# Kernel optimization log

Hardware: AMD Instinct MI355X
Metric: run time of the kernel (lower is better)

## Reference

```python
import jax, jax.numpy as jnp
import numpy as np

B, NQ, NK, D, DV = 8, 2048, 2048, 64, 64
MASK_VAL = -1e9  # any value < -1.0 triggers substitution in the original t.where


def setup_inputs() -> dict:
    key = jax.random.key(0)
    kq, kk, kv = jax.random.split(key, 3)
    queries = jax.random.normal(kq, (B, NQ, D), dtype=jnp.float32)
    keys = jax.random.normal(kk, (B, NK, D), dtype=jnp.float32)
    values = jax.random.normal(kv, (B, NK, DV), dtype=jnp.float32)
    # causal-style substitution mask: 0.0 where attended, -1e9 where masked
    causal = jnp.tril(jnp.ones((NQ, NK), dtype=jnp.float32))
    mask2d = jnp.where(causal > 0, 0.0, MASK_VAL)
    attention_mask = jnp.broadcast_to(mask2d, (B, NQ, NK))
    return {"queries": queries, "keys": keys, "values": values,
            "attention_mask": attention_mask}


def reference(queries, keys, values, attention_mask):
    # logits = Q K^T / sqrt(d_k)
    d_k = keys.shape[-1]
    scale = jnp.asarray(1.0 / np.sqrt(d_k), dtype=queries.dtype)
    logits = jnp.einsum('bqd,bkd->bqk', queries, keys) * scale
    # substitution masking: replace logits by the mask VALUE where mask < -1.0
    masked = jnp.where(attention_mask < -1.0, attention_mask, logits)
    attn = jax.nn.softmax(masked, axis=-1)
    # post-hoc NaN zeroing (rows fully masked with -inf would be NaN)
    attn = jnp.where(jnp.isnan(attn), jnp.asarray(0.0, attn.dtype), attn)
    return jnp.einsum('bqk,bkv->bqv', attn, values)
```

## Files before the change

### kernel.cpp

```cpp
#include <hip/hip_runtime.h>

#define NB    8
#define NQL   2048
#define NKL   2048
#define DD    64
#define DVV   64
#define QT    64
#define NQT   32
#define KSTEP 64
#define PPB   119
#define MAXCH 7

typedef __attribute__((ext_vector_type(8))) short bf16x8;
typedef __attribute__((ext_vector_type(4))) short bf16x4;
typedef __attribute__((ext_vector_type(2))) short bf16x2;
typedef __attribute__((ext_vector_type(4))) float f32x4;

#define L2E 1.44269504088896340736f

__device__ __forceinline__ unsigned short f2bf(float x) {
    union { float f; unsigned u; } v; v.f = x;
    unsigned r = v.u + 0x7FFFu + ((v.u >> 16) & 1u);
    return (unsigned short)(r >> 16);
}

__device__ __forceinline__ int kswz(int row, int col) {
    return row * 64 + (col ^ ((row & 7) << 3));
}
__device__ __forceinline__ int vswz(int dv, int col) {
    return dv * 64 + (col ^ ((((dv & 7) ^ ((dv >> 3) & 7))) << 3));
}

__global__ __launch_bounds__(256, 4)
void attn_part(const float* __restrict__ Qg, const float* __restrict__ Kg,
               const float* __restrict__ Vg, float* __restrict__ Og,
               float* __restrict__ Mp, float* __restrict__ Lp,
               float* __restrict__ Op)
{
    const int bid = blockIdx.x;
    const int b   = bid / PPB;
    const int r   = bid - b * PPB;
    int qt = 0, P = 1, j = 0;
    {
        int cum = 0;
#pragma unroll
        for (int t = 0; t < 32; ++t) {
            int pc = (t + 5) / 5;
            if (r >= cum && r < cum + pc) { qt = t; P = pc; j = r - cum; }
            cum += pc;
        }
    }
    const int n    = qt + 1;
    const int base = n / P;
    const int rem  = n - base * P;
    const int s0   = j * base + (j < rem ? j : rem);
    const int nsteps = base + (j < rem ? 1 : 0);
    const int KC0  = s0 * KSTEP;
    const int pidx = b * PPB + r;

    const int tid  = threadIdx.x;
    const int wv   = tid >> 6;
    const int lane = tid & 63;
    const int c    = lane & 15;
    const int h    = lane >> 4;
    const int Q0   = qt * QT;
    const int R0l  = 16 * wv;

    const float* Qb = Qg + (size_t)b * NQL * DD;
    const float* Kb = Kg + (size_t)b * NKL * DD;
    const float* Vb = Vg + (size_t)b * NKL * DVV;

    __shared__ short Kl[2][64 * 64];
    __shared__ short Vl[2][64 * 64];

    const int skr = tid >> 2;
    const int sdc = (tid & 3) * 16;
    const int vkr = (tid >> 3) << 1;
    const int vdc = (tid & 7) * 8;
    f32x4 kr[4], vr[4];

    bf16x8 qf[2];
#pragma unroll
    for (int dh = 0; dh < 2; ++dh) {
        const float* src = Qb + (size_t)(Q0 + R0l + c) * DD + dh * 32 + h * 8;
        f32x4 x0 = *(const f32x4*)(src);
        f32x4 x1 = *(const f32x4*)(src + 4);
        bf16x8 t;
#pragma unroll
        for (int jj = 0; jj < 4; ++jj) {
            t[jj]     = (short)f2bf(x0[jj] * 0.125f);
            t[4 + jj] = (short)f2bf(x1[jj] * 0.125f);
        }
        qf[dh] = t;
    }

    {
        const float* kb0 = Kb + (size_t)(KC0 + skr) * DD + sdc;
        kr[0] = *(const f32x4*)(kb0);     kr[1] = *(const f32x4*)(kb0 + 4);
        kr[2] = *(const f32x4*)(kb0 + 8); kr[3] = *(const f32x4*)(kb0 + 12);
        const float* vb0 = Vb + (size_t)(KC0 + vkr) * DVV + vdc;
        vr[0] = *(const f32x4*)(vb0);       vr[1] = *(const f32x4*)(vb0 + 4);
        vr[2] = *(const f32x4*)(vb0 + DVV); vr[3] = *(const f32x4*)(vb0 + DVV + 4);
        short* Kd = Kl[0]; short* Vd = Vl[0];
#pragma unroll
        for (int i = 0; i < 4; ++i) {
            bf16x4 t;
#pragma unroll
            for (int jj = 0; jj < 4; ++jj) t[jj] = (short)f2bf(kr[i][jj]);
            *(bf16x4*)(Kd + kswz(skr, sdc + 4 * i)) = t;
        }
#pragma unroll
        for (int jj = 0; jj < 8; ++jj) {
            bf16x2 t;
            t[0] = (short)f2bf(vr[jj >> 2][jj & 3]);
            t[1] = (short)f2bf(vr[2 + (jj >> 2)][jj & 3]);
            *(bf16x2*)(Vd + vswz(vdc + jj, vkr)) = t;
        }
    }
    __syncthreads();

    float m = -INFINITY, l = 0.0f;
    f32x4 acc[4];
    {
        f32x4 z = {0.f, 0.f, 0.f, 0.f};
#pragma unroll
        for (int s4 = 0; s4 < 4; ++s4) acc[s4] = z;
    }

    for (int s = 0; s < nsteps; ++s) {
        const int pb = s & 1;

        if (s + 1 < nsteps) {
            const float* kb0 = Kb + (size_t)(KC0 + (s + 1) * KSTEP + skr) * DD + sdc;
            kr[0] = *(const f32x4*)(kb0);     kr[1] = *(const f32x4*)(kb0 + 4);
            kr[2] = *(const f32x4*)(kb0 + 8); kr[3] = *(const f32x4*)(kb0 + 12);
            const float* vb0 = Vb + (size_t)(KC0 + (s + 1) * KSTEP + vkr) * DVV + vdc;
            vr[0] = *(const f32x4*)(vb0);       vr[1] = *(const f32x4*)(vb0 + 4);
            vr[2] = *(const f32x4*)(vb0 + DVV); vr[3] = *(const f32x4*)(vb0 + DVV + 4);
        }

        const int kg0 = KC0 + s * KSTEP;
        if (kg0 <= Q0 + R0l + 15) {
            const short* Kd = Kl[pb];
            const short* Vd = Vl[pb];

            f32x4 st[4];
            {
                f32x4 z = {0.f, 0.f, 0.f, 0.f};
#pragma unroll
                for (int t = 0; t < 4; ++t) st[t] = z;
            }
            __builtin_amdgcn_s_setprio(1);
#pragma unroll
            for (int t = 0; t < 4; ++t)
#pragma unroll
                for (int dh = 0; dh < 2; ++dh) {
                    bf16x8 kf = *(const bf16x8*)(Kd + kswz(16 * t + c, dh * 32 + h * 8));
                    st[t] = __builtin_amdgcn_mfma_f32_16x16x32_bf16(kf, qf[dh], st[t], 0, 0, 0);
                }
            __builtin_amdgcn_s_setprio(0);

            if (kg0 + KSTEP - 1 > Q0 + R0l) {
                const int qg = Q0 + R0l + c;
#pragma unroll
                for (int t = 0; t < 4; ++t)
#pragma unroll
                    for (int rr = 0; rr < 4; ++rr) {
                        int key = kg0 + 16 * t + 4 * h + rr;
                        if (key > qg) st[t][rr] = -1e9f;
                    }
            }

            float vmax = st[0][0];
#pragma unroll
            for (int t = 0; t < 4; ++t)
#pragma unroll
                for (int rr = 0; rr < 4; ++rr) vmax = fmaxf(vmax, st[t][rr]);
            vmax = fmaxf(vmax, __shfl_xor(vmax, 16));
            vmax = fmaxf(vmax, __shfl_xor(vmax, 32));

            if (!__all(vmax - m <= 8.0f)) {
                float mn    = fmaxf(m, vmax);
                float alpha = exp2f((m - mn) * L2E);
                l *= alpha;
#pragma unroll
                for (int s4 = 0; s4 < 4; ++s4)
#pragma unroll
                    for (int rr = 0; rr < 4; ++rr) acc[s4][rr] *= alpha;
                m = mn;
            }

            float p[4][4];
            float ps = 0.f;
#pragma unroll
            for (int t = 0; t < 4; ++t)
#pragma unroll
                for (int rr = 0; rr < 4; ++rr) {
                    p[t][rr] = exp2f((st[t][rr] - m) * L2E);
                    ps += p[t][rr];
                }
            ps += __shfl_xor(ps, 16);
            ps += __shfl_xor(ps, 32);
            l += ps;

            bf16x8 pf[2];
#pragma unroll
            for (int u = 0; u < 2; ++u) {
                bf16x8 t;
#pragma unroll
                for (int jj = 0; jj < 8; ++jj) t[jj] = (short)f2bf(p[2 * u + (jj >> 2)][jj & 3]);
                pf[u] = t;
            }
            __builtin_amdgcn_s_setprio(1);
#pragma unroll
            for (int s4 = 0; s4 < 4; ++s4)
#pragma unroll
                for (int u = 0; u < 2; ++u) {
                    bf16x4 lo = *(const bf16x4*)(Vd + vswz(c + 16 * s4, 32 * u + 4 * h));
                    bf16x4 hi = *(const bf16x4*)(Vd + vswz(c + 16 * s4, 32 * u + 16 + 4 * h));
                    bf16x8 vf = {lo[0], lo[1], lo[2], lo[3], hi[0], hi[1], hi[2], hi[3]};
                    acc[s4] = __builtin_amdgcn_mfma_f32_16x16x32_bf16(vf, pf[u], acc[s4], 0, 0, 0);
                }
            __builtin_amdgcn_s_setprio(0);
        }

        if (s + 1 < nsteps) {
            short* Kd = Kl[(s + 1) & 1];
            short* Vd = Vl[(s + 1) & 1];
#pragma unroll
            for (int i = 0; i < 4; ++i) {
                bf16x4 t;
#pragma unroll
                for (int jj = 0; jj < 4; ++jj) t[jj] = (short)f2bf(kr[i][jj]);
                *(bf16x4*)(Kd + kswz(skr, sdc + 4 * i)) = t;
            }
#pragma unroll
            for (int jj = 0; jj < 8; ++jj) {
                bf16x2 t;
                t[0] = (short)f2bf(vr[jj >> 2][jj & 3]);
                t[1] = (short)f2bf(vr[2 + (jj >> 2)][jj & 3]);
                *(bf16x2*)(Vd + vswz(vdc + jj, vkr)) = t;
            }
            __syncthreads();
        }
    }

    const int q = R0l + c;
    if (P == 1) {
        const float iv = 1.0f / l;
        float* dst = Og + ((size_t)b * NQL + Q0 + q) * DVV;
#pragma unroll
        for (int s4 = 0; s4 < 4; ++s4) {
            f32x4 t = acc[s4];
#pragma unroll
            for (int rr = 0; rr < 4; ++rr) t[rr] *= iv;
            *(f32x4*)(dst + 16 * s4 + 4 * h) = t;
        }
        return;
    }

    float* Opg = Op + (size_t)pidx * (QT * DVV);
#pragma unroll
    for (int s4 = 0; s4 < 4; ++s4)
        *(f32x4*)(Opg + (size_t)q * DVV + 16 * s4 + 4 * h) = acc[s4];
    if (h == 0) {
        Mp[(size_t)pidx * QT + q] = m;
        Lp[(size_t)pidx * QT + q] = l;
    }
}

__global__ __launch_bounds__(256)
void attn_comb(const float* __restrict__ Op, const float* __restrict__ Mp,
               const float* __restrict__ Lp, float* __restrict__ Og)
{
    const int seg = blockIdx.x & 1;
    const int t2  = blockIdx.x >> 1;
    const int b   = t2 / 27;
    const int qt  = 5 + (t2 - b * 27);
    const int nch = (qt + 5) / 5;
    int rbase = 0;
#pragma unroll
    for (int t = 0; t < 32; ++t) if (t < qt) rbase += (t + 5) / 5;
    const size_t p0 = (size_t)(b * PPB + rbase);

    const int tid = threadIdx.x;
    const int r0  = seg * 32;

    __shared__ float scb[MAXCH][32];

    if (tid < 32) {
        const int row = r0 + tid;
        float M = -INFINITY;
        for (int ch = 0; ch < nch; ++ch)
            M = fmaxf(M, Mp[(p0 + ch) * QT + row]);
        float den = 0.f;
        for (int ch = 0; ch < nch; ++ch) {
            float e = exp2f((Mp[(p0 + ch) * QT + row] - M) * L2E);
            den += e * Lp[(p0 + ch) * QT + row];
            scb[ch][tid] = e;
        }
        float iv = 1.0f / den;
        for (int ch = 0; ch < nch; ++ch) scb[ch][tid] *= iv;
    }
    __syncthreads();

    const float* Opt = Op + p0 * (QT * DVV) + (size_t)r0 * DVV;
    float* dst = Og + ((size_t)b * NQL + qt * QT + r0) * DVV;
#pragma unroll
    for (int jj = 0; jj < 8; ++jj) {
        int f = jj * 256 + tid;
        int row = f >> 6;
        float val = 0.f;
        for (int ch = 0; ch < nch; ++ch)
            val += scb[ch][row] * Opt[(size_t)ch * (QT * DVV) + f];
        dst[f] = val;
    }
}

__global__ __launch_bounds__(256, 4)
void attn_fwd_fb(const float* __restrict__ Qg, const float* __restrict__ Kg,
                 const float* __restrict__ Vg, float* __restrict__ Og)
{
    const int tid  = threadIdx.x;
    const int wv   = tid >> 6;
    const int lane = tid & 63;
    const int c    = lane & 15;
    const int h    = lane >> 4;
    const int bid = blockIdx.x;
    const int b   = bid & 7;
    const int qt  = bid >> 3;
    const int q0  = qt << 4;
    const float* Qb = Qg + (size_t)b * NQL * DD;
    const float* Kb = Kg + (size_t)b * NKL * DD;
    const float* Vb = Vg + (size_t)b * NKL * DVV;
    bf16x8 qf[2];
#pragma unroll
    for (int dh = 0; dh < 2; ++dh) {
        const float* src = Qb + (size_t)(q0 + c) * DD + dh * 32 + h * 8;
        f32x4 x0 = *(const f32x4*)(src);
        f32x4 x1 = *(const f32x4*)(src + 4);
        bf16x8 t;
#pragma unroll
        for (int jj = 0; jj < 4; ++jj) {
            t[jj]     = (short)f2bf(x0[jj] * 0.125f);
            t[4 + jj] = (short)f2bf(x1[jj] * 0.125f);
        }
        qf[dh] = t;
    }
    float m = -INFINITY, l = 0.0f;
    f32x4 acc[4];
    {
        f32x4 z = {0.f, 0.f, 0.f, 0.f};
#pragma unroll
        for (int s = 0; s < 4; ++s) acc[s] = z;
    }
    const int nkt = (q0 + 47) >> 5;
    for (int kt = wv; kt < nkt; kt += 4) {
        const int kb = kt << 5;
        f32x4 st[2];
        {
            f32x4 z = {0.f, 0.f, 0.f, 0.f};
            st[0] = z; st[1] = z;
        }
#pragma unroll
        for (int t = 0; t < 2; ++t)
#pragma unroll
            for (int dh = 0; dh < 2; ++dh) {
                const float* src = Kb + (size_t)(kb + t * 16 + c) * DD + dh * 32 + h * 8;
                f32x4 x0 = *(const f32x4*)(src);
                f32x4 x1 = *(const f32x4*)(src + 4);
                bf16x8 kf;
#pragma unroll
                for (int jj = 0; jj < 4; ++jj) {
                    kf[jj]     = (short)f2bf(x0[jj]);
                    kf[4 + jj] = (short)f2bf(x1[jj]);
                }
                st[t] = __builtin_amdgcn_mfma_f32_16x16x32_bf16(kf, qf[dh], st[t], 0, 0, 0);
            }
        if (kb + 31 > q0) {
#pragma unroll
            for (int t = 0; t < 2; ++t)
#pragma unroll
                for (int rr = 0; rr < 4; ++rr) {
                    int key = kb + t * 16 + h * 4 + rr;
                    if (key > q0 + c) st[t][rr] = -1e9f;
                }
        }
        float vmax = st[0][0];
#pragma unroll
        for (int t = 0; t < 2; ++t)
#pragma unroll
            for (int rr = 0; rr < 4; ++rr) vmax = fmaxf(vmax, st[t][rr]);
        vmax = fmaxf(vmax, __shfl_xor(vmax, 16));
        vmax = fmaxf(vmax, __shfl_xor(vmax, 32));
        float mn    = fmaxf(m, vmax);
        float alpha = exp2f((m - mn) * L2E);
        float p[2][4];
        float ps = 0.f;
#pragma unroll
        for (int t = 0; t < 2; ++t)
#pragma unroll
            for (int rr = 0; rr < 4; ++rr) {
                p[t][rr] = exp2f((st[t][rr] - mn) * L2E);
                ps += p[t][rr];
            }
        ps += __shfl_xor(ps, 16);
        ps += __shfl_xor(ps, 32);
        l = l * alpha + ps;
        m = mn;
#pragma unroll
        for (int s = 0; s < 4; ++s)
#pragma unroll
            for (int rr = 0; rr < 4; ++rr) acc[s][rr] *= alpha;
        bf16x8 pf;
#pragma unroll
        for (int jj = 0; jj < 8; ++jj) pf[jj] = (short)f2bf(p[jj >> 2][jj & 3]);
        size_t vrow[8];
#pragma unroll
        for (int jj = 0; jj < 8; ++jj)
            vrow[jj] = (size_t)(kb + h * 4 + (jj & 3) + ((jj >> 2) << 4)) * DVV + c;
#pragma unroll
        for (int s = 0; s < 4; ++s) {
            bf16x8 vf;
#pragma unroll
            for (int jj = 0; jj < 8; ++jj) vf[jj] = (short)f2bf(Vb[vrow[jj] + s * 16]);
            acc[s] = __builtin_amdgcn_mfma_f32_16x16x32_bf16(vf, pf, acc[s], 0, 0, 0);
        }
    }
    __shared__ float Osc[4][64][17];
    __shared__ float Msc[4][16];
    __shared__ float Lsc[4][16];
#pragma unroll
    for (int s = 0; s < 4; ++s)
#pragma unroll
        for (int rr = 0; rr < 4; ++rr)
            Osc[wv][s * 16 + h * 4 + rr][c] = acc[s][rr];
    if (lane < 16) { Msc[wv][c] = m; Lsc[wv][c] = l; }
    __syncthreads();
#pragma unroll
    for (int ri = 0; ri < 4; ++ri) {
        const int q = wv * 4 + ri;
        float M = fmaxf(fmaxf(Msc[0][q], Msc[1][q]), fmaxf(Msc[2][q], Msc[3][q]));
        float val = 0.f, den = 0.f;
#pragma unroll
        for (int w2 = 0; w2 < 4; ++w2) {
            float sc = exp2f((Msc[w2][q] - M) * L2E);
            den += Lsc[w2][q] * sc;
            val += Osc[w2][lane][q] * sc;
        }
        Og[((size_t)b * NQL + q0 + q) * DVV + lane] = val / den;
    }
}

extern "C" void kernel_launch(void* const* d_in, const int* in_sizes, int n_in,
                              void* d_out, int out_size, void* d_ws, size_t ws_size,
                              hipStream_t stream)
{
    (void)in_sizes; (void)n_in; (void)out_size;
    const float* Q = (const float*)d_in[0];
    const float* K = (const float*)d_in[1];
    const float* V = (const float*)d_in[2];
    float* O = (float*)d_out;

    const size_t npieces  = (size_t)NB * PPB;
    const size_t ml_elems = npieces * QT;
    const size_t op_elems = npieces * QT * DVV;
    const size_t need = (2 * ml_elems + op_elems) * sizeof(float);

    if (ws_size >= need) {
        float* Mp = (float*)d_ws;
        float* Lp = Mp + ml_elems;
        float* Op = Lp + ml_elems;
        attn_part<<<dim3(NB * PPB), dim3(256), 0, stream>>>(
            Q, K, V, O, Mp, Lp, Op);
        attn_comb<<<dim3(NB * 27 * 2), dim3(256), 0, stream>>>(Op, Mp, Lp, O);
    } else {
        attn_fwd_fb<<<dim3(NB * (NQL / 16)), dim3(256), 0, stream>>>(Q, K, V, O);
    }
}
```

Baseline: 50.12 us.

## Pre-convert K/V to bf16 (V transposed) and deepen register prefetch pipeline

Adds a pre-pass kernel that converts K to bf16 and transposes V to bf16 in workspace, so the attention kernel loads half as many bytes per tile and skips per-tile conversion and scattered V stores. The main loop is fully unrolled to a max of 5 steps with a two-stage register prefetch, and explicit vmcnt/lgkmcnt waits plus raw barriers replace __syncthreads. This adds an extra kernel launch and a full pass over K/V each call. It also relies on hand-placed waitcnt instructions being correct.

Measured after the change: 49.95 us. Within noise of the previous version (-0.3%).

```diff
diff --git a/kernel.cpp b/kernel.cpp
--- a/kernel.cpp
+++ b/kernel.cpp
@@ -10,13 +10,18 @@
 #define KSTEP 64
 #define PPB   119
 #define MAXCH 7
+#define MAXST 5
 
 typedef __attribute__((ext_vector_type(8))) short bf16x8;
 typedef __attribute__((ext_vector_type(4))) short bf16x4;
-typedef __attribute__((ext_vector_type(2))) short bf16x2;
+typedef __attribute__((ext_vector_type(8))) unsigned short u16x8;
 typedef __attribute__((ext_vector_type(4))) float f32x4;
 
 #define L2E 1.44269504088896340736f
+
+#define VMCNT4 asm volatile("s_waitcnt vmcnt(4)" ::: "memory")
+#define VMCNT0 asm volatile("s_waitcnt vmcnt(0)" ::: "memory")
+#define LGKM0  asm volatile("s_waitcnt lgkmcnt(0)" ::: "memory")
 
 __device__ __forceinline__ unsigned short f2bf(float x) {
     union { float f; unsigned u; } v; v.f = x;
@@ -31,9 +36,47 @@
     return dv * 64 + (col ^ ((((dv & 7) ^ ((dv >> 3) & 7))) << 3));
 }
 
+__global__ __launch_bounds__(256)
+void cvt_kv(const float* __restrict__ K, const float* __restrict__ V,
+            unsigned short* __restrict__ Kw, unsigned short* __restrict__ Vt)
+{
+    const int bid = blockIdx.x;
+    if (bid < 512) {
+        size_t i = ((size_t)bid * 256 + threadIdx.x) * 8;
+        f32x4 a = *(const f32x4*)(K + i);
+        f32x4 b = *(const f32x4*)(K + i + 4);
+        u16x8 o;
+#pragma unroll
+        for (int j = 0; j < 4; ++j) { o[j] = f2bf(a[j]); o[4 + j] = f2bf(b[j]); }
+        *(u16x8*)(Kw + i) = o;
+    } else {
+        const int v  = bid - 512;
+        const int b  = v >> 5;
+        const int k0 = (v & 31) << 6;
+        __shared__ float tile[64][65];
+        const float* Vb = V + ((size_t)b * NKL + k0) * DVV;
+        const int col = threadIdx.x & 63;
+        const int r4  = threadIdx.x >> 6;
+#pragma unroll
+        for (int i = 0; i < 16; ++i) {
+            int r = i * 4 + r4;
+            tile[r][col] = Vb[(size_t)r * DVV + col];
+        }
+        __syncthreads();
+        unsigned short* Vtb = Vt + (size_t)b * DVV * NKL;
+#pragma unroll
+        for (int i = 0; i < 16; ++i) {
+            int dv = i * 4 + r4;
+            Vtb[(size_t)dv * NKL + k0 + col] = f2bf(tile[col][dv]);
+        }
+    }
+}
+
 __global__ __launch_bounds__(256, 4)
-void attn_part(const float* __restrict__ Qg, const float* __restrict__ Kg,
-               const float* __restrict__ Vg, float* __restrict__ Og,
+void attn_part(const float* __restrict__ Qg,
+               const unsigned short* __restrict__ Kw,
+               const unsigned short* __restrict__ Vt,
+               float* __restrict__ Og,
                float* __restrict__ Mp, float* __restrict__ Lp,
                float* __restrict__ Op)
 {
@@ -50,13 +93,13 @@
             cum += pc;
         }
     }
-    const int n    = qt + 1;
-    const int base = n / P;
-    const int rem  = n - base * P;
-    const int s0   = j * base + (j < rem ? j : rem);
+    const int n      = qt + 1;
+    const int base   = n / P;
+    const int rem    = n - base * P;
+    const int s0     = j * base + (j < rem ? j : rem);
     const int nsteps = base + (j < rem ? 1 : 0);
-    const int KC0  = s0 * KSTEP;
-    const int pidx = b * PPB + r;
+    const int KC0    = s0 * KSTEP;
+    const int pidx   = b * PPB + r;
 
     const int tid  = threadIdx.x;
     const int wv   = tid >> 6;
@@ -66,18 +109,33 @@
     const int Q0   = qt * QT;
     const int R0l  = 16 * wv;
 
-    const float* Qb = Qg + (size_t)b * NQL * DD;
-    const float* Kb = Kg + (size_t)b * NKL * DD;
-    const float* Vb = Vg + (size_t)b * NKL * DVV;
+    const float*          Qb  = Qg + (size_t)b * NQL * DD;
+    const unsigned short* Kwb = Kw + (size_t)b * NKL * DD;
+    const unsigned short* Vtb = Vt + (size_t)b * DVV * NKL;
 
     __shared__ short Kl[2][64 * 64];
     __shared__ short Vl[2][64 * 64];
 
-    const int skr = tid >> 2;
-    const int sdc = (tid & 3) * 16;
-    const int vkr = (tid >> 3) << 1;
-    const int vdc = (tid & 7) * 8;
-    f32x4 kr[4], vr[4];
+    const int skr  = tid >> 2;
+    const int sc16 = (tid & 3) * 16;
+
+    struct Stage { bf16x8 k0, k1, v0, v1; };
+    Stage rg[2];
+
+    auto ISSUE = [&](int s, int pi) {
+        const unsigned short* kp = Kwb + (size_t)(KC0 + s * KSTEP + skr) * 64 + sc16;
+        rg[pi].k0 = *(const bf16x8*)(kp);
+        rg[pi].k1 = *(const bf16x8*)(kp + 8);
+        const unsigned short* vp = Vtb + (size_t)skr * NKL + KC0 + s * KSTEP + sc16;
+        rg[pi].v0 = *(const bf16x8*)(vp);
+        rg[pi].v1 = *(const bf16x8*)(vp + 8);
+    };
+    auto WRITE = [&](int pi, int buf) {
+        *(bf16x8*)(&Kl[buf][0] + kswz(skr, sc16))     = rg[pi].k0;
+        *(bf16x8*)(&Kl[buf][0] + kswz(skr, sc16 + 8)) = rg[pi].k1;
+        *(bf16x8*)(&Vl[buf][0] + vswz(skr, sc16))     = rg[pi].v0;
+        *(bf16x8*)(&Vl[buf][0] + vswz(skr, sc16 + 8)) = rg[pi].v1;
+    };
 
     bf16x8 qf[2];
 #pragma unroll
@@ -94,30 +152,11 @@
         qf[dh] = t;
     }
 
-    {
-        const float* kb0 = Kb + (size_t)(KC0 + skr) * DD + sdc;
-        kr[0] = *(const f32x4*)(kb0);     kr[1] = *(const f32x4*)(kb0 + 4);
-        kr[2] = *(const f32x4*)(kb0 + 8); kr[3] = *(const f32x4*)(kb0 + 12);
-        const float* vb0 = Vb + (size_t)(KC0 + vkr) * DVV + vdc;
-        vr[0] = *(const f32x4*)(vb0);       vr[1] = *(const f32x4*)(vb0 + 4);
-        vr[2] = *(const f32x4*)(vb0 + DVV); vr[3] = *(const f32x4*)(vb0 + DVV + 4);
-        short* Kd = Kl[0]; short* Vd = Vl[0];
-#pragma unroll
-        for (int i = 0; i < 4; ++i) {
-            bf16x4 t;
-#pragma unroll
-            for (int jj = 0; jj < 4; ++jj) t[jj] = (short)f2bf(kr[i][jj]);
-            *(bf16x4*)(Kd + kswz(skr, sdc + 4 * i)) = t;
-        }
-#pragma unroll
-        for (int jj = 0; jj < 8; ++jj) {
-            bf16x2 t;
-            t[0] = (short)f2bf(vr[jj >> 2][jj & 3]);
-            t[1] = (short)f2bf(vr[2 + (jj >> 2)][jj & 3]);
-            *(bf16x2*)(Vd + vswz(vdc + jj, vkr)) = t;
-        }
-    }
-    __syncthreads();
+    ISSUE(0, 0);
+    if (nsteps > 1) { ISSUE(1, 1); VMCNT4; } else { VMCNT0; }
+    WRITE(0, 0);
+    LGKM0;
+    __builtin_amdgcn_s_barrier();
 
     float m = -INFINITY, l = 0.0f;
     f32x4 acc[4];
@@ -127,121 +166,102 @@
         for (int s4 = 0; s4 < 4; ++s4) acc[s4] = z;
     }
 
-    for (int s = 0; s < nsteps; ++s) {
-        const int pb = s & 1;
-
-        if (s + 1 < nsteps) {
-            const float* kb0 = Kb + (size_t)(KC0 + (s + 1) * KSTEP + skr) * DD + sdc;
-            kr[0] = *(const f32x4*)(kb0);     kr[1] = *(const f32x4*)(kb0 + 4);
-            kr[2] = *(const f32x4*)(kb0 + 8); kr[3] = *(const f32x4*)(kb0 + 12);
-            const float* vb0 = Vb + (size_t)(KC0 + (s + 1) * KSTEP + vkr) * DVV + vdc;
-            vr[0] = *(const f32x4*)(vb0);       vr[1] = *(const f32x4*)(vb0 + 4);
-            vr[2] = *(const f32x4*)(vb0 + DVV); vr[3] = *(const f32x4*)(vb0 + DVV + 4);
-        }
-
-        const int kg0 = KC0 + s * KSTEP;
-        if (kg0 <= Q0 + R0l + 15) {
-            const short* Kd = Kl[pb];
-            const short* Vd = Vl[pb];
-
-            f32x4 st[4];
-            {
-                f32x4 z = {0.f, 0.f, 0.f, 0.f};
-#pragma unroll
-                for (int t = 0; t < 4; ++t) st[t] = z;
+#pragma unroll
+    for (int s = 0; s < MAXST; ++s) {
+        if (s < nsteps) {
+            if (s + 2 < nsteps) ISSUE(s + 2, s & 1);
+
+            const int kg0 = KC0 + s * KSTEP;
+            if (kg0 <= Q0 + R0l + 15) {
+                const short* Kd = &Kl[s & 1][0];
+                const short* Vd = &Vl[s & 1][0];
+
+                f32x4 st[4];
+                {
+                    f32x4 z = {0.f, 0.f, 0.f, 0.f};
+#pragma unroll
+                    for (int t = 0; t < 4; ++t) st[t] = z;
+                }
+                __builtin_amdgcn_s_setprio(1);
+#pragma unroll
+                for (int t = 0; t < 4; ++t)
+#pragma unroll
+                    for (int dh = 0; dh < 2; ++dh) {
+                        bf16x8 kf = *(const bf16x8*)(Kd + kswz(16 * t + c, dh * 32 + h * 8));
+                        st[t] = __builtin_amdgcn_mfma_f32_16x16x32_bf16(kf, qf[dh], st[t], 0, 0, 0);
+                    }
+                __builtin_amdgcn_s_setprio(0);
+
+                if (kg0 + KSTEP - 1 > Q0 + R0l) {
+                    const int qg = Q0 + R0l + c;
+#pragma unroll
+                    for (int t = 0; t < 4; ++t)
+#pragma unroll
+                        for (int rr = 0; rr < 4; ++rr) {
+                            int key = kg0 + 16 * t + 4 * h + rr;
+                            if (key > qg) st[t][rr] = -1e9f;
+                        }
+                }
+
+                float vmax = st[0][0];
+#pragma unroll
+                for (int t = 0; t < 4; ++t)
+#pragma unroll
+                    for (int rr = 0; rr < 4; ++rr) vmax = fmaxf(vmax, st[t][rr]);
+                vmax = fmaxf(vmax, __shfl_xor(vmax, 16));
+                vmax = fmaxf(vmax, __shfl_xor(vmax, 32));
+
+                if (!__all(vmax - m <= 8.0f)) {
+                    float mn    = fmaxf(m, vmax);
+                    float alpha = exp2f((m - mn) * L2E);
+                    l *= alpha;
+#pragma unroll
+                    for (int s4 = 0; s4 < 4; ++s4)
+#pragma unroll
+                        for (int rr = 0; rr < 4; ++rr) acc[s4][rr] *= alpha;
+                    m = mn;
+                }
+
+                float p[4][4];
+                float ps = 0.f;
+#pragma unroll
+                for (int t = 0; t < 4; ++t)
+#pragma unroll
+                    for (int rr = 0; rr < 4; ++rr) {
+                        p[t][rr] = exp2f((st[t][rr] - m) * L2E);
+                        ps += p[t][rr];
+                    }
+                ps += __shfl_xor(ps, 16);
+                ps += __shfl_xor(ps, 32);
+                l += ps;
+
+                bf16x8 pf[2];
+#pragma unroll
+                for (int u = 0; u < 2; ++u) {
+                    bf16x8 t;
+#pragma unroll
+                    for (int jj = 0; jj < 8; ++jj) t[jj] = (short)f2bf(p[2 * u + (jj >> 2)][jj & 3]);
+                    pf[u] = t;
+                }
+                __builtin_amdgcn_s_setprio(1);
+#pragma unroll
+                for (int s4 = 0; s4 < 4; ++s4)
+#pragma unroll
+                    for (int u = 0; u < 2; ++u) {
+                        bf16x4 lo = *(const bf16x4*)(Vd + vswz(c + 16 * s4, 32 * u + 4 * h));
+                        bf16x4 hi = *(const bf16x4*)(Vd + vswz(c + 16 * s4, 32 * u + 16 + 4 * h));
+                        bf16x8 vf = {lo[0], lo[1], lo[2], lo[3], hi[0], hi[1], hi[2], hi[3]};
+                        acc[s4] = __builtin_amdgcn_mfma_f32_16x16x32_bf16(vf, pf[u], acc[s4], 0, 0, 0);
+                    }
+                __builtin_amdgcn_s_setprio(0);
             }
-            __builtin_amdgcn_s_setprio(1);
-#pragma unroll
-            for (int t = 0; t < 4; ++t)
-#pragma unroll
-                for (int dh = 0; dh < 2; ++dh) {
-                    bf16x8 kf = *(const bf16x8*)(Kd + kswz(16 * t + c, dh * 32 + h * 8));
-                    st[t] = __builtin_amdgcn_mfma_f32_16x16x32_bf16(kf, qf[dh], st[t], 0, 0, 0);
-                }
-            __builtin_amdgcn_s_setprio(0);
-
-            if (kg0 + KSTEP - 1 > Q0 + R0l) {
-                const int qg = Q0 + R0l + c;
-#pragma unroll
-                for (int t = 0; t < 4; ++t)
-#pragma unroll
-                    for (int rr = 0; rr < 4; ++rr) {
-                        int key = kg0 + 16 * t + 4 * h + rr;
-                        if (key > qg) st[t][rr] = -1e9f;
-                    }
+
+            if (s + 1 < nsteps) {
+                if (s + 2 < nsteps) { VMCNT4; } else { VMCNT0; }
+                WRITE((s + 1) & 1, (s + 1) & 1);
+                LGKM0;
+                __builtin_amdgcn_s_barrier();
             }
-
-            float vmax = st[0][0];
-#pragma unroll
-            for (int t = 0; t < 4; ++t)
-#pragma unroll
-                for (int rr = 0; rr < 4; ++rr) vmax = fmaxf(vmax, st[t][rr]);
-            vmax = fmaxf(vmax, __shfl_xor(vmax, 16));
-            vmax = fmaxf(vmax, __shfl_xor(vmax, 32));
-
-            if (!__all(vmax - m <= 8.0f)) {
-                float mn    = fmaxf(m, vmax);
-                float alpha = exp2f((m - mn) * L2E);
-                l *= alpha;
-#pragma unroll
-                for (int s4 = 0; s4 < 4; ++s4)
-#pragma unroll
-                    for (int rr = 0; rr < 4; ++rr) acc[s4][rr] *= alpha;
-                m = mn;
-            }
-
-            float p[4][4];
-            float ps = 0.f;
-#pragma unroll
-            for (int t = 0; t < 4; ++t)
-#pragma unroll
-                for (int rr = 0; rr < 4; ++rr) {
-                    p[t][rr] = exp2f((st[t][rr] - m) * L2E);
-                    ps += p[t][rr];
-                }
-            ps += __shfl_xor(ps, 16);
-            ps += __shfl_xor(ps, 32);
-            l += ps;
-
-            bf16x8 pf[2];
-#pragma unroll
-            for (int u = 0; u < 2; ++u) {
-                bf16x8 t;
-#pragma unroll
-                for (int jj = 0; jj < 8; ++jj) t[jj] = (short)f2bf(p[2 * u + (jj >> 2)][jj & 3]);
-                pf[u] = t;
-            }
-            __builtin_amdgcn_s_setprio(1);
-#pragma unroll
-            for (int s4 = 0; s4 < 4; ++s4)
-#pragma unroll
-                for (int u = 0; u < 2; ++u) {
-                    bf16x4 lo = *(const bf16x4*)(Vd + vswz(c + 16 * s4, 32 * u + 4 * h));
-                    bf16x4 hi = *(const bf16x4*)(Vd + vswz(c + 16 * s4, 32 * u + 16 + 4 * h));
-                    bf16x8 vf = {lo[0], lo[1], lo[2], lo[3], hi[0], hi[1], hi[2], hi[3]};
-                    acc[s4] = __builtin_amdgcn_mfma_f32_16x16x32_bf16(vf, pf[u], acc[s4], 0, 0, 0);
-                }
-            __builtin_amdgcn_s_setprio(0);
-        }
-
-        if (s + 1 < nsteps) {
-            short* Kd = Kl[(s + 1) & 1];
-            short* Vd = Vl[(s + 1) & 1];
-#pragma unroll
-            for (int i = 0; i < 4; ++i) {
-                bf16x4 t;
-#pragma unroll
-                for (int jj = 0; jj < 4; ++jj) t[jj] = (short)f2bf(kr[i][jj]);
-                *(bf16x4*)(Kd + kswz(skr, sdc + 4 * i)) = t;
-            }
-#pragma unroll
-            for (int jj = 0; jj < 8; ++jj) {
-                bf16x2 t;
-                t[0] = (short)f2bf(vr[jj >> 2][jj & 3]);
-                t[1] = (short)f2bf(vr[2 + (jj >> 2)][jj & 3]);
-                *(bf16x2*)(Vd + vswz(vdc + jj, vkr)) = t;
-            }
-            __syncthreads();
         }
     }
 
@@ -465,14 +485,19 @@
     const size_t npieces  = (size_t)NB * PPB;
     const size_t ml_elems = npieces * QT;
     const size_t op_elems = npieces * QT * DVV;
-    const size_t need = (2 * ml_elems + op_elems) * sizeof(float);
+    const size_t kv_elems = (size_t)NB * NKL * DD;
+    const size_t need = (2 * ml_elems + op_elems) * sizeof(float)
+                      + 2 * kv_elems * sizeof(unsigned short);
 
     if (ws_size >= need) {
         float* Mp = (float*)d_ws;
         float* Lp = Mp + ml_elems;
         float* Op = Lp + ml_elems;
+        unsigned short* Kw = (unsigned short*)(Op + op_elems);
+        unsigned short* Vt = Kw + kv_elems;
+        cvt_kv<<<dim3(768), dim3(256), 0, stream>>>(K, V, Kw, Vt);
         attn_part<<<dim3(NB * PPB), dim3(256), 0, stream>>>(
-            Q, K, V, O, Mp, Lp, Op);
+            Q, Kw, Vt, O, Mp, Lp, Op);
         attn_comb<<<dim3(NB * 27 * 2), dim3(256), 0, stream>>>(Op, Mp, Lp, O);
     } else {
         attn_fwd_fb<<<dim3(NB * (NQL / 16)), dim3(256), 0, stream>>>(Q, K, V, O);
```
